# Optimization experiments

Hardware: AMD Instinct MI355X
Metric: run time of the kernel (lower is better)

Reference implementation:

```python
import jax, jax.numpy as jnp
import numpy as np

RING_WORLD_SIZE = 4  # number of ring steps / KV sequence chunks


def _ring_flash_attention(q, k, v, ring_size):
    # q,k,v: [B, S, H, D]; non-causal full attention computed blockwise over
    # KV chunks (one per ring step) with numerically-stable online LSE merge,
    # mirroring _compact_ring_fwd + update_out_and_lse.
    B, S, H, D = q.shape
    scale = D ** (-0.5)
    chunk = S // ring_size
    out = None  # [B, S, H, D] accumulated in fp32
    lse = None  # [B, H, S] running log-sum-exp
    for step in range(ring_size):
        k_blk = jax.lax.dynamic_slice_in_dim(k, step * chunk, chunk, axis=1)
        v_blk = jax.lax.dynamic_slice_in_dim(v, step * chunk, chunk, axis=1)
        # scores: [B, H, Sq, Sk_blk]
        scores = jnp.einsum('bqhd,bkhd->bhqk', q, k_blk) * scale
        block_lse = jax.scipy.special.logsumexp(scores, axis=-1)  # [B,H,Sq]
        probs = jnp.exp(scores - block_lse[..., None])
        block_out = jnp.einsum('bhqk,bkhd->bqhd', probs, v_blk)
        if out is None:
            out, lse = block_out, block_lse
        else:
            new_lse = jnp.logaddexp(lse, block_lse)
            w_old = jnp.exp(lse - new_lse)       # [B,H,Sq]
            w_new = jnp.exp(block_lse - new_lse)
            # broadcast weights to [B,Sq,H,1]
            out = (jnp.transpose(w_old, (0, 2, 1))[..., None] * out
                   + jnp.transpose(w_new, (0, 2, 1))[..., None] * block_out)
            lse = new_lse
    return out.astype(q.dtype)


def setup_inputs() -> dict:
    key = jax.random.key(0)
    kq, kk, kv = jax.random.split(key, 3)
    shape = (1, 4096, 16, 128)
    return {
        'query': jax.random.normal(kq, shape, dtype=jnp.float32),
        'key': jax.random.normal(kk, shape, dtype=jnp.float32),
        'value': jax.random.normal(kv, shape, dtype=jnp.float32),
    }


def reference(query, key, value):
    # Ulysses all-to-all is identity on a single logical device; the ring loop
    # with lossless (error-feedback) KV compression reduces to blockwise
    # attention with online softmax merging.
    return _ring_flash_attention(query, key, value, RING_WORLD_SIZE)
```

## Files before the change

### kernel.cpp

```cpp
#include <hip/hip_runtime.h>
#include <hip/hip_bf16.h>

#define S_LEN 4096
#define NH    16
#define DD    128
#define HD    2048
#define QB    128
#define KB    64
#define NT    (S_LEN/KB)

typedef __bf16 bf16_t;
typedef bf16_t bf16x8 __attribute__((ext_vector_type(8)));
typedef float  f32x4  __attribute__((ext_vector_type(4)));

static __device__ __forceinline__ bf16x8 pack8(float4 a, float4 b, float s) {
  bf16x8 v;
  v[0]=(bf16_t)(a.x*s); v[1]=(bf16_t)(a.y*s); v[2]=(bf16_t)(a.z*s); v[3]=(bf16_t)(a.w*s);
  v[4]=(bf16_t)(b.x*s); v[5]=(bf16_t)(b.y*s); v[6]=(bf16_t)(b.z*s); v[7]=(bf16_t)(b.w*s);
  return v;
}

static __device__ __forceinline__ void gload_lds16(const void* g, void* l) {
  __builtin_amdgcn_global_load_lds((const __attribute__((address_space(1))) void*)g,
                                   (__attribute__((address_space(3))) void*)l, 16, 0, 0);
}

__global__ __launch_bounds__(256) void prep_k(const float* __restrict__ Kg,
                                              bf16_t* __restrict__ Kp) {
  const int kt = blockIdx.x, h = blockIdx.y, tid = threadIdx.x;
  __shared__ bf16_t tile[KB][DD + 8];
  #pragma unroll
  for (int it = 0; it < 8; ++it) {
    int lin4 = it*256 + tid;
    int r  = lin4 >> 5;
    int dc = (lin4 & 31) * 4;
    float4 a = *(const float4*)(Kg + (size_t)(kt*KB + r)*HD + h*DD + dc);
    tile[r][dc+0]=(bf16_t)a.x; tile[r][dc+1]=(bf16_t)a.y;
    tile[r][dc+2]=(bf16_t)a.z; tile[r][dc+3]=(bf16_t)a.w;
  }
  __syncthreads();
  bf16_t* out = Kp + (size_t)(h*NT + kt)*8192;
  #pragma unroll
  for (int it = 0; it < 4; ++it) {
    int cid = it*256 + tid;
    int f = cid >> 6, l = cid & 63;
    int b = f >> 2, c = f & 3;
    int row = b*16 + (l & 15);
    int d0  = c*32 + (l >> 4)*8;
    bf16x8 v = *(const bf16x8*)(&tile[row][d0]);
    *(bf16x8*)(out + (size_t)cid*8) = v;
  }
}

__global__ __launch_bounds__(256) void prep_v(const float* __restrict__ Vg,
                                              bf16_t* __restrict__ Vp) {
  const int kt = blockIdx.x, h = blockIdx.y, tid = threadIdx.x;
  __shared__ bf16_t tile[KB][DD + 8];
  #pragma unroll
  for (int it = 0; it < 8; ++it) {
    int lin4 = it*256 + tid;
    int r  = lin4 >> 5;
    int dc = (lin4 & 31) * 4;
    float4 a = *(const float4*)(Vg + (size_t)(kt*KB + r)*HD + h*DD + dc);
    tile[r][dc+0]=(bf16_t)a.x; tile[r][dc+1]=(bf16_t)a.y;
    tile[r][dc+2]=(bf16_t)a.z; tile[r][dc+3]=(bf16_t)a.w;
  }
  __syncthreads();
  bf16_t* out = Vp + (size_t)(h*NT + kt)*8192;
  #pragma unroll
  for (int it = 0; it < 4; ++it) {
    int cid = it*256 + tid;
    int f = cid >> 6, l = cid & 63;
    int ks = f >> 3, db = f & 7;
    int d  = db*16 + (l & 15);
    int c0 = ks*32 + (l >> 4)*8;
    bf16x8 v;
    #pragma unroll
    for (int m = 0; m < 8; ++m) {
      int c = c0 + m;
      int k = 32*(c>>5) + 16*((c>>2)&1) + 4*((c>>3)&3) + (c&3);
      v[m] = tile[k][d];
    }
    *(bf16x8*)(out + (size_t)cid*8) = v;
  }
}

__global__ __launch_bounds__(256, 3) void attn_fwd(const float* __restrict__ Qg,
                                                   const bf16_t* __restrict__ Kp,
                                                   const bf16_t* __restrict__ Vp,
                                                   float* __restrict__ Og) {
  const int phys = blockIdx.x;
  const int logical = (phys & 7) * 64 + (phys >> 3);
  const int h  = logical >> 5;
  const int qt = logical & 31;
  const int tid  = threadIdx.x;
  const int wid  = tid >> 6;
  const int lane = tid & 63;
  const int l16  = lane & 15;
  const int lg   = lane >> 4;
  const int lo16 = lane * 16;

  __shared__ alignas(16) bf16_t Ks[8192];
  __shared__ alignas(16) bf16_t Vt[2][8192];

  const float qs = 0.08838834764831845f * 1.4426950408889634f;
  bf16x8 qf[2][4];
  #pragma unroll
  for (int g = 0; g < 2; ++g) {
    const int qrow = qt*QB + wid*32 + g*16 + l16;
    const float* qp = Qg + (size_t)qrow*HD + h*DD + lg*8;
    #pragma unroll
    for (int c = 0; c < 4; ++c) {
      float4 a = *(const float4*)(qp + c*32);
      float4 b = *(const float4*)(qp + c*32 + 4);
      qf[g][c] = pack8(a, b, qs);
    }
  }
  bf16x8 onesf;
  #pragma unroll
  for (int j = 0; j < 8; ++j) onesf[j] = (bf16_t)1.0f;
  asm volatile("" ::: "memory");

  const int lo = tid*16;
  auto issueK = [&](int kt) {
    const char* kg = (const char*)(Kp + (size_t)(h*NT + kt)*8192);
    char* kl = (char*)&Ks[0];
    #pragma unroll
    for (int p = 0; p < 4; ++p) gload_lds16(kg + lo + p*4096, kl + lo + p*4096);
  };
  auto issueV = [&](int kt) {
    const char* vg = (const char*)(Vp + (size_t)(h*NT + kt)*8192);
    char* vl = (char*)&Vt[kt & 1][0];
    #pragma unroll
    for (int p = 0; p < 4; ++p) gload_lds16(vg + lo + p*4096, vl + lo + p*4096);
  };

  f32x4 acc[2][8];
  f32x4 acc_l[2];
  #pragma unroll
  for (int g = 0; g < 2; ++g) {
    #pragma unroll
    for (int i = 0; i < 8; ++i) acc[g][i] = (f32x4){0.f,0.f,0.f,0.f};
    acc_l[g] = (f32x4){0.f,0.f,0.f,0.f};
  }
  float m_run[2] = {-__builtin_inff(), -__builtin_inff()};

  issueK(0);
  issueV(0);

  for (int kt = 0; kt < NT; ++kt) {
    const int cur = kt & 1;
    asm volatile("s_waitcnt vmcnt(0) lgkmcnt(0)" ::: "memory");
    __builtin_amdgcn_sched_barrier(0);
    __builtin_amdgcn_s_barrier();

    if (kt + 1 < NT) issueV(kt + 1);

    f32x4 sc[2][4];
    #pragma unroll
    for (int g = 0; g < 2; ++g)
      #pragma unroll
      for (int b = 0; b < 4; ++b) sc[g][b] = (f32x4){0.f,0.f,0.f,0.f};
    {
      const char* KsB = (const char*)&Ks[0] + lo16;
      __builtin_amdgcn_s_setprio(1);
      #pragma unroll
      for (int b = 0; b < 4; ++b) {
        #pragma unroll
        for (int c = 0; c < 4; ++c) {
          bf16x8 kb = *(const bf16x8*)(KsB + ((b*4 + c) << 10));
          sc[0][b] = __builtin_amdgcn_mfma_f32_16x16x32_bf16(kb, qf[0][c], sc[0][b], 0, 0, 0);
          sc[1][b] = __builtin_amdgcn_mfma_f32_16x16x32_bf16(kb, qf[1][c], sc[1][b], 0, 0, 0);
        }
      }
      __builtin_amdgcn_s_setprio(0);
    }

    asm volatile("s_waitcnt lgkmcnt(0)" ::: "memory");
    __builtin_amdgcn_sched_barrier(0);
    __builtin_amdgcn_s_barrier();
    if (kt + 1 < NT) issueK(kt + 1);

    bf16x8 pp[2][2];
    #pragma unroll
    for (int g = 0; g < 2; ++g) {
      float pmax;
      {
        float a0 = fmaxf(fmaxf(sc[g][0][0], sc[g][0][1]), sc[g][0][2]);
        float a1 = fmaxf(fmaxf(sc[g][0][3], sc[g][1][0]), sc[g][1][1]);
        float a2 = fmaxf(fmaxf(sc[g][1][2], sc[g][1][3]), sc[g][2][0]);
        float a3 = fmaxf(fmaxf(sc[g][2][1], sc[g][2][2]), sc[g][2][3]);
        float a4 = fmaxf(fmaxf(sc[g][3][0], sc[g][3][1]), sc[g][3][2]);
        float b0 = fmaxf(fmaxf(a0, a1), a2);
        float b1 = fmaxf(fmaxf(a3, a4), sc[g][3][3]);
        pmax = fmaxf(b0, b1);
      }
      if (!__all(pmax - m_run[g] <= 8.0f)) {
        pmax = fmaxf(pmax, __shfl_xor(pmax, 16));
        pmax = fmaxf(pmax, __shfl_xor(pmax, 32));
        float mnew  = fmaxf(m_run[g], pmax);
        float alpha = exp2f(m_run[g] - mnew);
        m_run[g] = mnew;
        #pragma unroll
        for (int i = 0; i < 8; ++i) {
          #pragma unroll
          for (int r = 0; r < 4; ++r) acc[g][i][r] *= alpha;
        }
        #pragma unroll
        for (int r = 0; r < 4; ++r) acc_l[g][r] *= alpha;
      }
      #pragma unroll
      for (int b = 0; b < 4; ++b) {
        #pragma unroll
        for (int r = 0; r < 4; ++r) {
          float p = exp2f(sc[g][b][r] - m_run[g]);
          pp[g][b >> 1][(b & 1)*4 + r] = (bf16_t)p;
        }
      }
    }

    {
      const char* VtB = (const char*)&Vt[cur][0] + lo16;
      __builtin_amdgcn_s_setprio(1);
      #pragma unroll
      for (int ks = 0; ks < 2; ++ks) {
        acc_l[0] = __builtin_amdgcn_mfma_f32_16x16x32_bf16(onesf, pp[0][ks], acc_l[0], 0, 0, 0);
        acc_l[1] = __builtin_amdgcn_mfma_f32_16x16x32_bf16(onesf, pp[1][ks], acc_l[1], 0, 0, 0);
        #pragma unroll
        for (int db = 0; db < 8; ++db) {
          bf16x8 va = *(const bf16x8*)(VtB + ((ks*8 + db) << 10));
          acc[0][db] = __builtin_amdgcn_mfma_f32_16x16x32_bf16(va, pp[0][ks], acc[0][db], 0, 0, 0);
          acc[1][db] = __builtin_amdgcn_mfma_f32_16x16x32_bf16(va, pp[1][ks], acc[1][db], 0, 0, 0);
        }
      }
      __builtin_amdgcn_s_setprio(0);
    }
  }

  #pragma unroll
  for (int g = 0; g < 2; ++g) {
    const int qrow = qt*QB + wid*32 + g*16 + l16;
    const float inv = 1.0f / acc_l[g][0];
    float* op = Og + (size_t)qrow*HD + h*DD + lg*4;
    #pragma unroll
    for (int db = 0; db < 8; ++db) {
      float4 o;
      o.x = acc[g][db][0]*inv; o.y = acc[g][db][1]*inv;
      o.z = acc[g][db][2]*inv; o.w = acc[g][db][3]*inv;
      *(float4*)(op + db*16) = o;
    }
  }
}

extern "C" void kernel_launch(void* const* d_in, const int* in_sizes, int n_in,
                              void* d_out, int out_size, void* d_ws, size_t ws_size,
                              hipStream_t stream) {
  const float* Q = (const float*)d_in[0];
  const float* K = (const float*)d_in[1];
  const float* V = (const float*)d_in[2];
  float* O = (float*)d_out;
  bf16_t* Kp = (bf16_t*)d_ws;
  bf16_t* Vp = Kp + (size_t)NH*S_LEN*DD;
  prep_k<<<dim3(NT, NH), 256, 0, stream>>>(K, Kp);
  prep_v<<<dim3(NT, NH), 256, 0, stream>>>(V, Vp);
  attn_fwd<<<dim3(512), 256, 0, stream>>>(Q, Kp, Vp, O);
}
```

Baseline: 189.0 us.

## Split KV range across two blocks per query tile and merge partials

Each query tile is now handled by two blocks, each covering half of the KV tiles, which doubles the attention grid from 512 to 1024 blocks. Each block writes an unnormalized partial output plus its row sum and running max. A new merge kernel combines the two partials using LSE weights and normalizes. The aim is better CU occupancy and less tail imbalance. The cost is extra global traffic for the partial outputs and statistics, one more kernel launch, and a larger workspace.

```diff
diff --git a/kernel.cpp b/kernel.cpp
--- a/kernel.cpp
+++ b/kernel.cpp
@@ -8,6 +8,7 @@
 #define QB    128
 #define KB    64
 #define NT    (S_LEN/KB)
+#define NTH   (NT/2)
 
 typedef __bf16 bf16_t;
 typedef bf16_t bf16x8 __attribute__((ext_vector_type(8)));
@@ -88,17 +89,22 @@
 __global__ __launch_bounds__(256, 3) void attn_fwd(const float* __restrict__ Qg,
                                                    const bf16_t* __restrict__ Kp,
                                                    const bf16_t* __restrict__ Vp,
-                                                   float* __restrict__ Og) {
+                                                   float* __restrict__ A0,
+                                                   float* __restrict__ A1,
+                                                   float* __restrict__ lmW) {
   const int phys = blockIdx.x;
-  const int logical = (phys & 7) * 64 + (phys >> 3);
-  const int h  = logical >> 5;
-  const int qt = logical & 31;
+  const int logical = (phys & 7) * 128 + (phys >> 3);
+  const int h   = logical >> 6;
+  const int rem = logical & 63;
+  const int qt  = rem >> 1;
+  const int p   = rem & 1;
   const int tid  = threadIdx.x;
   const int wid  = tid >> 6;
   const int lane = tid & 63;
   const int l16  = lane & 15;
   const int lg   = lane >> 4;
   const int lo16 = lane * 16;
+  const int kt0 = p * NTH;
 
   __shared__ alignas(16) bf16_t Ks[8192];
   __shared__ alignas(16) bf16_t Vt[2][8192];
@@ -126,13 +132,13 @@
     const char* kg = (const char*)(Kp + (size_t)(h*NT + kt)*8192);
     char* kl = (char*)&Ks[0];
     #pragma unroll
-    for (int p = 0; p < 4; ++p) gload_lds16(kg + lo + p*4096, kl + lo + p*4096);
+    for (int pp2 = 0; pp2 < 4; ++pp2) gload_lds16(kg + lo + pp2*4096, kl + lo + pp2*4096);
   };
   auto issueV = [&](int kt) {
     const char* vg = (const char*)(Vp + (size_t)(h*NT + kt)*8192);
     char* vl = (char*)&Vt[kt & 1][0];
     #pragma unroll
-    for (int p = 0; p < 4; ++p) gload_lds16(vg + lo + p*4096, vl + lo + p*4096);
+    for (int pp2 = 0; pp2 < 4; ++pp2) gload_lds16(vg + lo + pp2*4096, vl + lo + pp2*4096);
   };
 
   f32x4 acc[2][8];
@@ -145,16 +151,16 @@
   }
   float m_run[2] = {-__builtin_inff(), -__builtin_inff()};
 
-  issueK(0);
-  issueV(0);
-
-  for (int kt = 0; kt < NT; ++kt) {
+  issueK(kt0);
+  issueV(kt0);
+
+  for (int kt = kt0; kt < kt0 + NTH; ++kt) {
     const int cur = kt & 1;
     asm volatile("s_waitcnt vmcnt(0) lgkmcnt(0)" ::: "memory");
     __builtin_amdgcn_sched_barrier(0);
     __builtin_amdgcn_s_barrier();
 
-    if (kt + 1 < NT) issueV(kt + 1);
+    if (kt + 1 < kt0 + NTH) issueV(kt + 1);
 
     f32x4 sc[2][4];
     #pragma unroll
@@ -179,7 +185,7 @@
     asm volatile("s_waitcnt lgkmcnt(0)" ::: "memory");
     __builtin_amdgcn_sched_barrier(0);
     __builtin_amdgcn_s_barrier();
-    if (kt + 1 < NT) issueK(kt + 1);
+    if (kt + 1 < kt0 + NTH) issueK(kt + 1);
 
     bf16x8 pp[2][2];
     #pragma unroll
@@ -213,8 +219,8 @@
       for (int b = 0; b < 4; ++b) {
         #pragma unroll
         for (int r = 0; r < 4; ++r) {
-          float p = exp2f(sc[g][b][r] - m_run[g]);
-          pp[g][b >> 1][(b & 1)*4 + r] = (bf16_t)p;
+          float pv = exp2f(sc[g][b][r] - m_run[g]);
+          pp[g][b >> 1][(b & 1)*4 + r] = (bf16_t)pv;
         }
       }
     }
@@ -237,19 +243,47 @@
     }
   }
 
+  float* Ap = p ? A1 : A0;
   #pragma unroll
   for (int g = 0; g < 2; ++g) {
     const int qrow = qt*QB + wid*32 + g*16 + l16;
-    const float inv = 1.0f / acc_l[g][0];
-    float* op = Og + (size_t)qrow*HD + h*DD + lg*4;
+    float* op = Ap + (size_t)qrow*HD + h*DD + lg*4;
     #pragma unroll
     for (int db = 0; db < 8; ++db) {
       float4 o;
-      o.x = acc[g][db][0]*inv; o.y = acc[g][db][1]*inv;
-      o.z = acc[g][db][2]*inv; o.w = acc[g][db][3]*inv;
+      o.x = acc[g][db][0]; o.y = acc[g][db][1];
+      o.z = acc[g][db][2]; o.w = acc[g][db][3];
       *(float4*)(op + db*16) = o;
     }
-  }
+    if (lg == 0) {
+      size_t row = (size_t)h*S_LEN + qrow;
+      lmW[(size_t)p*131072 + row]         = acc_l[g][0];
+      lmW[(size_t)p*131072 + 65536 + row] = m_run[g];
+    }
+  }
+}
+
+__global__ __launch_bounds__(256) void merge2(const float* __restrict__ A1,
+                                              const float* __restrict__ lmW,
+                                              float* __restrict__ O) {
+  size_t idx = (size_t)blockIdx.x*256 + threadIdx.x;
+  size_t sh = idx >> 5;
+  int hh = (int)(sh & 15);
+  int ss = (int)(sh >> 4);
+  size_t row = (size_t)hh*S_LEN + ss;
+  float l0 = lmW[row],          m0 = lmW[65536 + row];
+  float l1 = lmW[131072 + row], m1 = lmW[196608 + row];
+  float m  = fmaxf(m0, m1);
+  float w0 = exp2f(m0 - m), w1 = exp2f(m1 - m);
+  float inv = 1.0f / (l0*w0 + l1*w1);
+  float4 a0 = *(const float4*)(O  + idx*4);
+  float4 a1 = *(const float4*)(A1 + idx*4);
+  float4 o;
+  o.x = (a0.x*w0 + a1.x*w1)*inv;
+  o.y = (a0.y*w0 + a1.y*w1)*inv;
+  o.z = (a0.z*w0 + a1.z*w1)*inv;
+  o.w = (a0.w*w0 + a1.w*w1)*inv;
+  *(float4*)(O + idx*4) = o;
 }
 
 extern "C" void kernel_launch(void* const* d_in, const int* in_sizes, int n_in,
@@ -260,8 +294,11 @@
   const float* V = (const float*)d_in[2];
   float* O = (float*)d_out;
   bf16_t* Kp = (bf16_t*)d_ws;
-  bf16_t* Vp = Kp + (size_t)NH*S_LEN*DD;
+  bf16_t* Vp = Kp + (size_t)8388608;
+  float*  A1 = (float*)(Vp + (size_t)8388608);
+  float*  lm = A1 + (size_t)8388608;
   prep_k<<<dim3(NT, NH), 256, 0, stream>>>(K, Kp);
   prep_v<<<dim3(NT, NH), 256, 0, stream>>>(V, Vp);
-  attn_fwd<<<dim3(512), 256, 0, stream>>>(Q, Kp, Vp, O);
-}
+  attn_fwd<<<dim3(1024), 256, 0, stream>>>(Q, Kp, Vp, O, A1, lm);
+  merge2<<<dim3(8192), 256, 0, stream>>>(A1, lm, O);
+}
```

New measurement: 193.2 us. 2.2% more time.

## Halve Q tile and KV sub-stage to double grid size and occupancy

Applied to the files above, without the earlier changes.

Each block now handles 64 query rows (one 16-row group per wave) instead of 128, and the KV loop streams 32-key half-tiles over 128 stages instead of 64-key tiles over 64 stages. The grid doubles to 1024 blocks, LDS per block halves, and launch bounds raise the target to 4 blocks per CU to improve occupancy and latency hiding. In exchange, each K/V byte loaded into LDS is reused by half as many query rows, so global/L2 traffic doubles. Per-stage barrier and wait overhead also doubles relative to the MFMA work done per stage.

```diff
diff --git a/kernel.cpp b/kernel.cpp
--- a/kernel.cpp
+++ b/kernel.cpp
@@ -5,9 +5,10 @@
 #define NH    16
 #define DD    128
 #define HD    2048
-#define QB    128
+#define QB    64
 #define KB    64
 #define NT    (S_LEN/KB)
+#define NS    128
 
 typedef __bf16 bf16_t;
 typedef bf16_t bf16x8 __attribute__((ext_vector_type(8)));
@@ -85,14 +86,14 @@
   }
 }
 
-__global__ __launch_bounds__(256, 3) void attn_fwd(const float* __restrict__ Qg,
+__global__ __launch_bounds__(256, 4) void attn_fwd(const float* __restrict__ Qg,
                                                    const bf16_t* __restrict__ Kp,
                                                    const bf16_t* __restrict__ Vp,
                                                    float* __restrict__ Og) {
   const int phys = blockIdx.x;
-  const int logical = (phys & 7) * 64 + (phys >> 3);
-  const int h  = logical >> 5;
-  const int qt = logical & 31;
+  const int logical = (phys & 7) * 128 + (phys >> 3);
+  const int h  = logical >> 6;
+  const int qt = logical & 63;
   const int tid  = threadIdx.x;
   const int wid  = tid >> 6;
   const int lane = tid & 63;
@@ -100,20 +101,19 @@
   const int lg   = lane >> 4;
   const int lo16 = lane * 16;
 
-  __shared__ alignas(16) bf16_t Ks[8192];
-  __shared__ alignas(16) bf16_t Vt[2][8192];
+  __shared__ alignas(16) bf16_t Ks[4096];
+  __shared__ alignas(16) bf16_t Vt[2][4096];
 
   const float qs = 0.08838834764831845f * 1.4426950408889634f;
-  bf16x8 qf[2][4];
-  #pragma unroll
-  for (int g = 0; g < 2; ++g) {
-    const int qrow = qt*QB + wid*32 + g*16 + l16;
+  bf16x8 qf[4];
+  {
+    const int qrow = qt*QB + wid*16 + l16;
     const float* qp = Qg + (size_t)qrow*HD + h*DD + lg*8;
     #pragma unroll
     for (int c = 0; c < 4; ++c) {
       float4 a = *(const float4*)(qp + c*32);
       float4 b = *(const float4*)(qp + c*32 + 4);
-      qf[g][c] = pack8(a, b, qs);
+      qf[c] = pack8(a, b, qs);
     }
   }
   bf16x8 onesf;
@@ -122,55 +122,51 @@
   asm volatile("" ::: "memory");
 
   const int lo = tid*16;
-  auto issueK = [&](int kt) {
-    const char* kg = (const char*)(Kp + (size_t)(h*NT + kt)*8192);
+  const char* KpH = (const char*)Kp + (size_t)h*1048576;
+  const char* VpH = (const char*)Vp + (size_t)h*1048576;
+  auto issueK = [&](int s) {
+    const char* kg = KpH + (size_t)s*8192;
     char* kl = (char*)&Ks[0];
-    #pragma unroll
-    for (int p = 0; p < 4; ++p) gload_lds16(kg + lo + p*4096, kl + lo + p*4096);
+    gload_lds16(kg + lo,        kl + lo);
+    gload_lds16(kg + lo + 4096, kl + lo + 4096);
   };
-  auto issueV = [&](int kt) {
-    const char* vg = (const char*)(Vp + (size_t)(h*NT + kt)*8192);
-    char* vl = (char*)&Vt[kt & 1][0];
-    #pragma unroll
-    for (int p = 0; p < 4; ++p) gload_lds16(vg + lo + p*4096, vl + lo + p*4096);
+  auto issueV = [&](int s) {
+    const char* vg = VpH + (size_t)s*8192;
+    char* vl = (char*)&Vt[s & 1][0];
+    gload_lds16(vg + lo,        vl + lo);
+    gload_lds16(vg + lo + 4096, vl + lo + 4096);
   };
 
-  f32x4 acc[2][8];
-  f32x4 acc_l[2];
-  #pragma unroll
-  for (int g = 0; g < 2; ++g) {
-    #pragma unroll
-    for (int i = 0; i < 8; ++i) acc[g][i] = (f32x4){0.f,0.f,0.f,0.f};
-    acc_l[g] = (f32x4){0.f,0.f,0.f,0.f};
-  }
-  float m_run[2] = {-__builtin_inff(), -__builtin_inff()};
+  f32x4 acc[8];
+  f32x4 acc_l;
+  #pragma unroll
+  for (int i = 0; i < 8; ++i) acc[i] = (f32x4){0.f,0.f,0.f,0.f};
+  acc_l = (f32x4){0.f,0.f,0.f,0.f};
+  float m_run = -__builtin_inff();
 
   issueK(0);
   issueV(0);
 
-  for (int kt = 0; kt < NT; ++kt) {
-    const int cur = kt & 1;
+  for (int s = 0; s < NS; ++s) {
+    const int cur = s & 1;
     asm volatile("s_waitcnt vmcnt(0) lgkmcnt(0)" ::: "memory");
     __builtin_amdgcn_sched_barrier(0);
     __builtin_amdgcn_s_barrier();
 
-    if (kt + 1 < NT) issueV(kt + 1);
-
-    f32x4 sc[2][4];
-    #pragma unroll
-    for (int g = 0; g < 2; ++g)
-      #pragma unroll
-      for (int b = 0; b < 4; ++b) sc[g][b] = (f32x4){0.f,0.f,0.f,0.f};
+    if (s + 1 < NS) issueV(s + 1);
+
+    f32x4 sc[2];
+    sc[0] = (f32x4){0.f,0.f,0.f,0.f};
+    sc[1] = (f32x4){0.f,0.f,0.f,0.f};
     {
       const char* KsB = (const char*)&Ks[0] + lo16;
       __builtin_amdgcn_s_setprio(1);
       #pragma unroll
-      for (int b = 0; b < 4; ++b) {
+      for (int b = 0; b < 2; ++b) {
         #pragma unroll
         for (int c = 0; c < 4; ++c) {
           bf16x8 kb = *(const bf16x8*)(KsB + ((b*4 + c) << 10));
-          sc[0][b] = __builtin_amdgcn_mfma_f32_16x16x32_bf16(kb, qf[0][c], sc[0][b], 0, 0, 0);
-          sc[1][b] = __builtin_amdgcn_mfma_f32_16x16x32_bf16(kb, qf[1][c], sc[1][b], 0, 0, 0);
+          sc[b] = __builtin_amdgcn_mfma_f32_16x16x32_bf16(kb, qf[c], sc[b], 0, 0, 0);
         }
       }
       __builtin_amdgcn_s_setprio(0);
@@ -179,42 +175,34 @@
     asm volatile("s_waitcnt lgkmcnt(0)" ::: "memory");
     __builtin_amdgcn_sched_barrier(0);
     __builtin_amdgcn_s_barrier();
-    if (kt + 1 < NT) issueK(kt + 1);
-
-    bf16x8 pp[2][2];
-    #pragma unroll
-    for (int g = 0; g < 2; ++g) {
-      float pmax;
-      {
-        float a0 = fmaxf(fmaxf(sc[g][0][0], sc[g][0][1]), sc[g][0][2]);
-        float a1 = fmaxf(fmaxf(sc[g][0][3], sc[g][1][0]), sc[g][1][1]);
-        float a2 = fmaxf(fmaxf(sc[g][1][2], sc[g][1][3]), sc[g][2][0]);
-        float a3 = fmaxf(fmaxf(sc[g][2][1], sc[g][2][2]), sc[g][2][3]);
-        float a4 = fmaxf(fmaxf(sc[g][3][0], sc[g][3][1]), sc[g][3][2]);
-        float b0 = fmaxf(fmaxf(a0, a1), a2);
-        float b1 = fmaxf(fmaxf(a3, a4), sc[g][3][3]);
-        pmax = fmaxf(b0, b1);
-      }
-      if (!__all(pmax - m_run[g] <= 8.0f)) {
+    if (s + 1 < NS) issueK(s + 1);
+
+    bf16x8 pp;
+    {
+      float t0 = fmaxf(fmaxf(sc[0][0], sc[0][1]), sc[0][2]);
+      float t1 = fmaxf(fmaxf(sc[0][3], sc[1][0]), sc[1][1]);
+      float t2 = fmaxf(sc[1][2], sc[1][3]);
+      float pmax = fmaxf(fmaxf(t0, t1), t2);
+      if (!__all(pmax - m_run <= 8.0f)) {
         pmax = fmaxf(pmax, __shfl_xor(pmax, 16));
         pmax = fmaxf(pmax, __shfl_xor(pmax, 32));
-        float mnew  = fmaxf(m_run[g], pmax);
-        float alpha = exp2f(m_run[g] - mnew);
-        m_run[g] = mnew;
+        float mnew  = fmaxf(m_run, pmax);
+        float alpha = exp2f(m_run - mnew);
+        m_run = mnew;
         #pragma unroll
         for (int i = 0; i < 8; ++i) {
           #pragma unroll
-          for (int r = 0; r < 4; ++r) acc[g][i][r] *= alpha;
+          for (int r = 0; r < 4; ++r) acc[i][r] *= alpha;
         }
         #pragma unroll
-        for (int r = 0; r < 4; ++r) acc_l[g][r] *= alpha;
+        for (int r = 0; r < 4; ++r) acc_l[r] *= alpha;
       }
       #pragma unroll
-      for (int b = 0; b < 4; ++b) {
+      for (int b = 0; b < 2; ++b) {
         #pragma unroll
         for (int r = 0; r < 4; ++r) {
-          float p = exp2f(sc[g][b][r] - m_run[g]);
-          pp[g][b >> 1][(b & 1)*4 + r] = (bf16_t)p;
+          float pv = exp2f(sc[b][r] - m_run);
+          pp[b*4 + r] = (bf16_t)pv;
         }
       }
     }
@@ -222,31 +210,25 @@
     {
       const char* VtB = (const char*)&Vt[cur][0] + lo16;
       __builtin_amdgcn_s_setprio(1);
+      acc_l = __builtin_amdgcn_mfma_f32_16x16x32_bf16(onesf, pp, acc_l, 0, 0, 0);
       #pragma unroll
-      for (int ks = 0; ks < 2; ++ks) {
-        acc_l[0] = __builtin_amdgcn_mfma_f32_16x16x32_bf16(onesf, pp[0][ks], acc_l[0], 0, 0, 0);
-        acc_l[1] = __builtin_amdgcn_mfma_f32_16x16x32_bf16(onesf, pp[1][ks], acc_l[1], 0, 0, 0);
-        #pragma unroll
-        for (int db = 0; db < 8; ++db) {
-          bf16x8 va = *(const bf16x8*)(VtB + ((ks*8 + db) << 10));
-          acc[0][db] = __builtin_amdgcn_mfma_f32_16x16x32_bf16(va, pp[0][ks], acc[0][db], 0, 0, 0);
-          acc[1][db] = __builtin_amdgcn_mfma_f32_16x16x32_bf16(va, pp[1][ks], acc[1][db], 0, 0, 0);
-        }
+      for (int db = 0; db < 8; ++db) {
+        bf16x8 va = *(const bf16x8*)(VtB + (db << 10));
+        acc[db] = __builtin_amdgcn_mfma_f32_16x16x32_bf16(va, pp, acc[db], 0, 0, 0);
       }
       __builtin_amdgcn_s_setprio(0);
     }
   }
 
-  #pragma unroll
-  for (int g = 0; g < 2; ++g) {
-    const int qrow = qt*QB + wid*32 + g*16 + l16;
-    const float inv = 1.0f / acc_l[g][0];
+  {
+    const int qrow = qt*QB + wid*16 + l16;
+    const float inv = 1.0f / acc_l[0];
     float* op = Og + (size_t)qrow*HD + h*DD + lg*4;
     #pragma unroll
     for (int db = 0; db < 8; ++db) {
       float4 o;
-      o.x = acc[g][db][0]*inv; o.y = acc[g][db][1]*inv;
-      o.z = acc[g][db][2]*inv; o.w = acc[g][db][3]*inv;
+      o.x = acc[db][0]*inv; o.y = acc[db][1]*inv;
+      o.z = acc[db][2]*inv; o.w = acc[db][3]*inv;
       *(float4*)(op + db*16) = o;
     }
   }
@@ -263,5 +245,5 @@
   bf16_t* Vp = Kp + (size_t)NH*S_LEN*DD;
   prep_k<<<dim3(NT, NH), 256, 0, stream>>>(K, Kp);
   prep_v<<<dim3(NT, NH), 256, 0, stream>>>(V, Vp);
-  attn_fwd<<<dim3(512), 256, 0, stream>>>(Q, Kp, Vp, O);
-}
+  attn_fwd<<<dim3(1024), 256, 0, stream>>>(Q, Kp, Vp, O);
+}
```

Result: slower. 196.4 us (+3.9%).
